# Performance work log

Hardware: AMD Instinct MI355X
Metric: run time of the kernel (lower is better)

Reference implementation:

```python
import jax, jax.numpy as jnp
import numpy as np

D = 768
H = 16
DH = D // H  # 48
SCALE = 1.0 / np.sqrt(DH).astype(np.float32)
EPS = 1e-3  # keras LayerNormalization default epsilon
NEG = -1e9


def setup_inputs() -> dict:
    key = jax.random.key(0)
    ks = jax.random.split(key, 10)
    B, S = 4, 2048
    q = jax.random.normal(ks[0], (B, S, D), dtype=jnp.float32)
    k = jax.random.normal(ks[1], (B, S, D), dtype=jnp.float32)
    v = jax.random.normal(ks[2], (B, S, D), dtype=jnp.float32)
    # Dense projection params (glorot-ish scale)
    w_std = 1.0 / np.sqrt(D)
    Wq = jax.random.normal(ks[3], (D, D), dtype=jnp.float32) * w_std
    Wk = jax.random.normal(ks[4], (D, D), dtype=jnp.float32) * w_std
    Wv = jax.random.normal(ks[5], (D, D), dtype=jnp.float32) * w_std
    bq = jnp.zeros((D,), jnp.float32)
    bk = jnp.zeros((D,), jnp.float32)
    bv = jnp.zeros((D,), jnp.float32)
    gamma = jnp.ones((D,), jnp.float32)
    beta = jnp.zeros((D,), jnp.float32)
    return {"q": q, "k": k, "v": v, "Wq": Wq, "bq": bq, "Wk": Wk, "bk": bk,
            "Wv": Wv, "bv": bv, "gamma": gamma, "beta": beta}


def reference(q, k, v, Wq, bq, Wk, bk, Wv, bv, gamma, beta):
    use_causal = True  # exercise the causal-mask path
    B, S, _ = q.shape
    # Projections, then split into heads (tf.split on last axis == reshape)
    Q = (q @ Wq + bq).reshape(B, S, H, DH)
    K = (k @ Wk + bk).reshape(B, S, H, DH)
    V = (v @ Wv + bv).reshape(B, S, H, DH)
    # scores: [B, H, Sq, Sk]
    scores = jnp.einsum('bqhd,bkhd->bhqk', Q, K) * SCALE
    if use_causal:
        qi = jnp.arange(S)[:, None]
        ki = jnp.arange(S)[None, :]
        mask = jnp.where(qi >= ki, 0.0, NEG).astype(scores.dtype)
        scores = scores + mask
    attn = jax.nn.softmax(scores, axis=-1)
    out = jnp.einsum('bhqk,bkhd->bqhd', attn, V).reshape(B, S, D)
    # LayerNorm over last dim
    mu = jnp.mean(out, axis=-1, keepdims=True)
    var = jnp.mean(jnp.square(out - mu), axis=-1, keepdims=True)
    return (out - mu) * jax.lax.rsqrt(var + EPS) * gamma + beta
```

## Files before the change

kernel.cpp:

```cpp
#include <hip/hip_runtime.h>
#include <hip/hip_bf16.h>


#define DMODEL 768
#define NHEAD  16
#define DHEAD  48
#define SEQ    2048
#define NBATCH 4
#define NROWS  (NBATCH * SEQ)
#define QSCALE (0.14433756729740643f * 1.4426950408889634f)

typedef __bf16 bf16x8 __attribute__((ext_vector_type(8)));
typedef float  f32x4  __attribute__((ext_vector_type(4)));

__global__ __launch_bounds__(256) void prep(
    const float* __restrict__ Wq,
    const float* __restrict__ Wk,
    const float* __restrict__ Wv,
    const float* __restrict__ xq,
    const float* __restrict__ xk,
    const float* __restrict__ xv,
    __hip_bfloat16* __restrict__ Wt,
    __hip_bfloat16* __restrict__ Xbq,
    __hip_bfloat16* __restrict__ Xbk,
    __hip_bfloat16* __restrict__ Xbv)
{
    int bid = blockIdx.x;
    if (bid < 1728) {
        __shared__ __hip_bfloat16 tile[32][33];
        int mat = bid / 576;
        int t   = bid - mat * 576;
        int tr  = t / 24, tc = t - (t / 24) * 24;
        const float* W = (mat == 0) ? Wq : (mat == 1) ? Wk : Wv;
        __hip_bfloat16* O = Wt + (size_t)mat * DMODEL * DMODEL;
        int tx = threadIdx.x & 31, ty = threadIdx.x >> 5;
#pragma unroll
        for (int i = 0; i < 32; i += 8)
            tile[ty + i][tx] = __float2bfloat16(W[(size_t)(tr * 32 + ty + i) * DMODEL + tc * 32 + tx]);
        __syncthreads();
#pragma unroll
        for (int i = 0; i < 32; i += 8)
            O[(size_t)(tc * 32 + ty + i) * DMODEL + tr * 32 + tx] = tile[tx][ty + i];
    } else {
        int b2  = bid - 1728;
        int mat = b2 / 3072;
        int r   = b2 - mat * 3072;
        const float* X = (mat == 0) ? xq : (mat == 1) ? xk : xv;
        __hip_bfloat16* O = (mat == 0) ? Xbq : (mat == 1) ? Xbk : Xbv;
        size_t off = (size_t)r * 2048 + threadIdx.x * 8;
        float4 f0 = *(const float4*)(X + off);
        float4 f1 = *(const float4*)(X + off + 4);
        union { __hip_bfloat16 h[8]; uint4 u; } pk;
        pk.h[0] = __float2bfloat16(f0.x); pk.h[1] = __float2bfloat16(f0.y);
        pk.h[2] = __float2bfloat16(f0.z); pk.h[3] = __float2bfloat16(f0.w);
        pk.h[4] = __float2bfloat16(f1.x); pk.h[5] = __float2bfloat16(f1.y);
        pk.h[6] = __float2bfloat16(f1.z); pk.h[7] = __float2bfloat16(f1.w);
        *(uint4*)(O + off) = pk.u;
    }
}

__global__ __launch_bounds__(512, 4) void qkv_proj(
    const __hip_bfloat16* __restrict__ Xbq,
    const __hip_bfloat16* __restrict__ Xbk,
    const __hip_bfloat16* __restrict__ Xbv,
    const __hip_bfloat16* __restrict__ Wt,
    const float* __restrict__ bq,
    const float* __restrict__ bk,
    const float* __restrict__ bv,
    __hip_bfloat16* __restrict__ Qr,
    __hip_bfloat16* __restrict__ Kr,
    __hip_bfloat16* __restrict__ Vt)
{
    __shared__ __hip_bfloat16 Abuf[3][8192];
    __shared__ __hip_bfloat16 Bbuf[2][4096];

    int tid  = threadIdx.x;
    int w    = tid >> 6, lane = tid & 63;
    int l16  = lane & 15, quad = lane >> 4;
    int wm   = w >> 1, wn = w & 1;

    int xcd = blockIdx.x & 7, s = blockIdx.x >> 3;
    int nt  = s % 6;
    int idx = (s / 6) * 8 + xcd;
    int mat = idx >> 5, mt = idx & 31;
    int m0  = mt * 256, n0 = nt * 128;

    const __hip_bfloat16* X = (mat == 0) ? Xbq : (mat == 1) ? Xbk : Xbv;
    const __hip_bfloat16* W = Wt + (size_t)mat * DMODEL * DMODEL;
    const float* bias       = (mat == 0) ? bq : (mat == 1) ? bk : bv;

    int sr = tid >> 2, sc = (tid & 3) * 8;
    const __hip_bfloat16* ga0 = X + (size_t)(m0 + sr) * DMODEL + sc;
    const __hip_bfloat16* ga1 = X + (size_t)(m0 + 128 + sr) * DMODEL + sc;
    const __hip_bfloat16* gb  = W + (size_t)(n0 + sr) * DMODEL + sc;

#define GLD(gp_, lp_) __builtin_amdgcn_global_load_lds(                        \
        (const __attribute__((address_space(1))) void*)(gp_),                  \
        (__attribute__((address_space(3))) void*)(lp_), 16, 0, 0)

    int aoff = (wm * 64 + l16) * 32 + quad * 8;
    int boff = (wn * 64 + l16) * 32 + quad * 8;

    f32x4 acc[4][4] = {};

    GLD(gb,       &Bbuf[0][tid * 8]);
    GLD(ga0,      &Abuf[0][tid * 8]);
    GLD(ga1,      &Abuf[0][4096 + tid * 8]);
    GLD(ga0 + 32, &Abuf[1][tid * 8]);
    GLD(ga1 + 32, &Abuf[1][4096 + tid * 8]);
    asm volatile("s_waitcnt vmcnt(2)" ::: "memory");
    asm volatile("s_barrier" ::: "memory");

    int abuf = 0, bbuf = 0, abS = 2;
    const __hip_bfloat16* gbS  = gb  + 32;
    const __hip_bfloat16* ga0S = ga0 + 64;
    const __hip_bfloat16* ga1S = ga1 + 64;

    for (int kt = 0; kt < 24; ++kt) {
        const __hip_bfloat16* LA = Abuf[abuf];
        const __hip_bfloat16* LB = Bbuf[bbuf];

        bf16x8 a[4], bA[2];
#pragma unroll
        for (int m_ = 0; m_ < 4; ++m_)
            a[m_] = *(const bf16x8*)&LA[aoff + m_ * 512];
        bA[0] = *(const bf16x8*)&LB[boff];
        bA[1] = *(const bf16x8*)&LB[boff + 512];

        if (kt < 23) { GLD(gbS, &Bbuf[bbuf ^ 1][tid * 8]); gbS += 32; }
        if (kt < 22) {
            GLD(ga0S, &Abuf[abS][tid * 8]);
            GLD(ga1S, &Abuf[abS][4096 + tid * 8]);
            ga0S += 32; ga1S += 32;
        }

        asm volatile("s_barrier" ::: "memory");
        __builtin_amdgcn_s_setprio(1);
#pragma unroll
        for (int m_ = 0; m_ < 4; ++m_) {
            acc[m_][0] = __builtin_amdgcn_mfma_f32_16x16x32_bf16(a[m_], bA[0], acc[m_][0], 0, 0, 0);
            acc[m_][1] = __builtin_amdgcn_mfma_f32_16x16x32_bf16(a[m_], bA[1], acc[m_][1], 0, 0, 0);
        }
        __builtin_amdgcn_s_setprio(0);
        asm volatile("s_barrier" ::: "memory");

        bf16x8 bB[2];
        bB[0] = *(const bf16x8*)&LB[boff + 1024];
        bB[1] = *(const bf16x8*)&LB[boff + 1536];

        if (kt < 22) asm volatile("s_waitcnt vmcnt(2)" ::: "memory");
        else         asm volatile("s_waitcnt vmcnt(0)" ::: "memory");
        asm volatile("s_barrier" ::: "memory");
        __builtin_amdgcn_s_setprio(1);
#pragma unroll
        for (int m_ = 0; m_ < 4; ++m_) {
            acc[m_][2] = __builtin_amdgcn_mfma_f32_16x16x32_bf16(a[m_], bB[0], acc[m_][2], 0, 0, 0);
            acc[m_][3] = __builtin_amdgcn_mfma_f32_16x16x32_bf16(a[m_], bB[1], acc[m_][3], 0, 0, 0);
        }
        __builtin_amdgcn_s_setprio(0);
        asm volatile("s_barrier" ::: "memory");

        abuf = (abuf == 2) ? 0 : abuf + 1;
        abS  = (abS  == 2) ? 0 : abS  + 1;
        bbuf ^= 1;
    }
#undef GLD

#pragma unroll
    for (int j = 0; j < 4; ++j) {
        int col = n0 + wn * 64 + j * 16 + l16;
        float bc = bias[col];
        if (mat == 0) {
#pragma unroll
            for (int i = 0; i < 4; ++i) {
                int row0 = m0 + wm * 64 + i * 16 + quad * 4;
#pragma unroll
                for (int r = 0; r < 4; ++r)
                    Qr[(size_t)(row0 + r) * DMODEL + col] =
                        __float2bfloat16((acc[i][j][r] + bc) * QSCALE);
            }
        } else if (mat == 1) {
#pragma unroll
            for (int i = 0; i < 4; ++i) {
                int row0 = m0 + wm * 64 + i * 16 + quad * 4;
#pragma unroll
                for (int r = 0; r < 4; ++r)
                    Kr[(size_t)(row0 + r) * DMODEL + col] =
                        __float2bfloat16(acc[i][j][r] + bc);
            }
        } else {
            int h = col / 48, dh = col - h * 48;
#pragma unroll
            for (int i = 0; i < 4; ++i) {
                int row0 = m0 + wm * 64 + i * 16 + quad * 4;
                int bb = row0 >> 11, s0 = row0 & 2047;
                ushort4 pk;
                union { __hip_bfloat16 b; unsigned short u; } cv;
                cv.b = __float2bfloat16(acc[i][j][0] + bc); pk.x = cv.u;
                cv.b = __float2bfloat16(acc[i][j][1] + bc); pk.y = cv.u;
                cv.b = __float2bfloat16(acc[i][j][2] + bc); pk.z = cv.u;
                cv.b = __float2bfloat16(acc[i][j][3] + bc); pk.w = cv.u;
                *(ushort4*)(Vt + ((size_t)(bb * NHEAD + h) * DHEAD + dh) * SEQ + s0) = pk;
            }
        }
    }
}

__global__ __launch_bounds__(256, 3) void attn(
    const __hip_bfloat16* __restrict__ Qr,
    const __hip_bfloat16* __restrict__ Kr,
    const __hip_bfloat16* __restrict__ Vt,
    __hip_bfloat16* __restrict__ Ao)
{
    __shared__ __hip_bfloat16 Ks[2][64][72];
    __shared__ __hip_bfloat16 Vs[2][48][72];
    __shared__ __hip_bfloat16 Ps[4][32][72];

    int tid  = threadIdx.x;
    int w    = tid >> 6, lane = tid & 63;
    int l16  = lane & 15, quad = lane >> 4;
    int bh   = blockIdx.x & 63;
    int qt   = 15 - (blockIdx.x >> 6);
    int q0   = qt * 128;
    int b    = bh >> 4, h = bh & 15;
    size_t rowbase = (size_t)b * SEQ;

    const __hip_bfloat16* Qp = Qr + rowbase * DMODEL + h * DHEAD;
    const __hip_bfloat16* Kp = Kr + rowbase * DMODEL + h * DHEAD;
    const __hip_bfloat16* Vp = Vt + (size_t)bh * DHEAD * SEQ;

    for (int idx = tid; idx < 1024; idx += 256) {
        int buf = idx >> 9, r = (idx >> 3) & 63, c = idx & 7;
        ((unsigned int*)&Ks[buf][r][48])[c] = 0u;
    }

    bf16x8 bQ0[2], bQ1[2];
#pragma unroll
    for (int i = 0; i < 2; ++i) {
        int qrow = q0 + w * 32 + i * 16 + l16;
        bQ0[i] = *(const bf16x8*)(Qp + (size_t)qrow * DMODEL + quad * 8);
        bQ1[i] = (bf16x8){};
        if (quad < 2)
            bQ1[i] = *(const bf16x8*)(Qp + (size_t)qrow * DMODEL + 32 + quad * 8);
    }

    int rK = tid >> 2, oK = (tid & 3) * 12;
    int dV = tid >> 3, oV = (tid & 7) * 8;

    uint2 kr0, kr1, kr2; uint4 vr0, vr1;

#define ATTN_LOAD(kt_) {                                                        \
        int k0_ = (kt_) * 64;                                                   \
        const __hip_bfloat16* kb_ = Kp + (size_t)(k0_ + rK) * DMODEL + oK;      \
        kr0 = *(const uint2*)(kb_);                                             \
        kr1 = *(const uint2*)(kb_ + 4);                                         \
        kr2 = *(const uint2*)(kb_ + 8);                                         \
        vr0 = *(const uint4*)(Vp + (size_t)dV * SEQ + k0_ + oV);                \
        if (tid < 128) vr1 = *(const uint4*)(Vp + (size_t)(32 + dV) * SEQ + k0_ + oV); }

#define ATTN_STORE(buf_) {                                                      \
        __hip_bfloat16* kd_ = &Ks[buf_][rK][oK];                                \
        *(uint2*)(kd_)     = kr0;                                               \
        *(uint2*)(kd_ + 4) = kr1;                                               \
        *(uint2*)(kd_ + 8) = kr2;                                               \
        *(uint4*)&Vs[buf_][dV][oV] = vr0;                                       \
        if (tid < 128) *(uint4*)&Vs[buf_][32 + dV][oV] = vr1; }

    f32x4 O[2][3] = {};
    float lsum[2] = {0.f, 0.f};

    int ktmax = 2 * qt + 1;
    ATTN_LOAD(0);
    ATTN_STORE(0);
    if (ktmax >= 1) ATTN_LOAD(1);
    __syncthreads();

    for (int kt = 0; kt <= ktmax; ++kt) {
        int buf = kt & 1;
        int k0  = kt * 64;
        if (kt + 1 <= ktmax) ATTN_STORE(buf ^ 1);
        if (kt + 2 <= ktmax) ATTN_LOAD(kt + 2);

        bf16x8 aK0[4], aK1[4];
#pragma unroll
        for (int t = 0; t < 4; ++t) {
            aK0[t] = *(const bf16x8*)&Ks[buf][16 * t + l16][quad * 8];
            aK1[t] = *(const bf16x8*)&Ks[buf][16 * t + l16][32 + quad * 8];
        }

#pragma unroll
        for (int i = 0; i < 2; ++i) {
            int qbase = q0 + w * 32 + i * 16;
            if (k0 > qbase + 15) continue;

            f32x4 s[4];
#pragma unroll
            for (int t = 0; t < 4; ++t) {
                f32x4 z = {};
                z    = __builtin_amdgcn_mfma_f32_16x16x32_bf16(aK0[t], bQ0[i], z, 0, 0, 0);
                s[t] = __builtin_amdgcn_mfma_f32_16x16x32_bf16(aK1[t], bQ1[i], z, 0, 0, 0);
            }

            if (k0 + 63 > qbase) {
                int qg = qbase + l16;
#pragma unroll
                for (int t = 0; t < 4; ++t) {
                    int kg = k0 + 16 * t + quad * 4;
#pragma unroll
                    for (int r = 0; r < 4; ++r)
                        if (kg + r > qg) s[t][r] = -1e30f;
                }
            }

            float ls = 0.f;
#pragma unroll
            for (int t = 0; t < 4; ++t) {
                float p0 = exp2f(s[t][0]), p1 = exp2f(s[t][1]);
                float p2 = exp2f(s[t][2]), p3 = exp2f(s[t][3]);
                ls += (p0 + p1) + (p2 + p3);
                union { __bf16 hv[4]; uint2 u2; } pk;
                pk.hv[0] = (__bf16)p0; pk.hv[1] = (__bf16)p1;
                pk.hv[2] = (__bf16)p2; pk.hv[3] = (__bf16)p3;
                *(uint2*)&Ps[w][i * 16 + l16][16 * t + quad * 4] = pk.u2;
            }
            lsum[i] += ls;
        }

        bf16x8 bV0[3], bV1[3];
#pragma unroll
        for (int dt = 0; dt < 3; ++dt) {
            bV0[dt] = *(const bf16x8*)&Vs[buf][dt * 16 + l16][quad * 8];
            bV1[dt] = *(const bf16x8*)&Vs[buf][dt * 16 + l16][32 + quad * 8];
        }

#pragma unroll
        for (int i = 0; i < 2; ++i) {
            int qbase = q0 + w * 32 + i * 16;
            if (k0 > qbase + 15) continue;
            bf16x8 aP0 = *(const bf16x8*)&Ps[w][i * 16 + l16][quad * 8];
            bf16x8 aP1 = *(const bf16x8*)&Ps[w][i * 16 + l16][32 + quad * 8];
#pragma unroll
            for (int dt = 0; dt < 3; ++dt) {
                O[i][dt] = __builtin_amdgcn_mfma_f32_16x16x32_bf16(aP0, bV0[dt], O[i][dt], 0, 0, 0);
                O[i][dt] = __builtin_amdgcn_mfma_f32_16x16x32_bf16(aP1, bV1[dt], O[i][dt], 0, 0, 0);
            }
        }

        asm volatile("s_waitcnt lgkmcnt(0)" ::: "memory");
        __builtin_amdgcn_s_barrier();
        asm volatile("" ::: "memory");
    }

#pragma unroll
    for (int i = 0; i < 2; ++i) {
        lsum[i] += __shfl_xor(lsum[i], 16, 64);
        lsum[i] += __shfl_xor(lsum[i], 32, 64);
    }

#pragma unroll
    for (int i = 0; i < 2; ++i) {
#pragma unroll
        for (int r = 0; r < 4; ++r) {
            float linv = 1.f / __shfl(lsum[i], quad * 4 + r, 64);
            size_t g = (rowbase + q0 + w * 32 + i * 16 + quad * 4 + r) * DMODEL + h * DHEAD + l16;
            Ao[g + 0]  = __float2bfloat16(O[i][0][r] * linv);
            Ao[g + 16] = __float2bfloat16(O[i][1][r] * linv);
            Ao[g + 32] = __float2bfloat16(O[i][2][r] * linv);
        }
    }
#undef ATTN_LOAD
#undef ATTN_STORE
}

__global__ __launch_bounds__(192) void lnorm(
    const __hip_bfloat16* __restrict__ Ao,
    const float* __restrict__ gamma,
    const float* __restrict__ beta,
    float* __restrict__ out)
{
    __shared__ float rs_[3], rq_[3];
    int row = blockIdx.x;
    int t   = threadIdx.x;
    size_t base = (size_t)row * DMODEL + t * 4;

    ushort4 u = *(const ushort4*)(Ao + base);
    float x0, x1, x2, x3;
    { unsigned int v = (unsigned int)u.x << 16; __builtin_memcpy(&x0, &v, 4); }
    { unsigned int v = (unsigned int)u.y << 16; __builtin_memcpy(&x1, &v, 4); }
    { unsigned int v = (unsigned int)u.z << 16; __builtin_memcpy(&x2, &v, 4); }
    { unsigned int v = (unsigned int)u.w << 16; __builtin_memcpy(&x3, &v, 4); }

    float s = x0 + x1 + x2 + x3;
    float q = x0 * x0 + x1 * x1 + x2 * x2 + x3 * x3;
#pragma unroll
    for (int m = 32; m >= 1; m >>= 1) {
        s += __shfl_xor(s, m, 64);
        q += __shfl_xor(q, m, 64);
    }
    int wv = t >> 6;
    if ((t & 63) == 0) { rs_[wv] = s; rq_[wv] = q; }
    __syncthreads();
    float ts = rs_[0] + rs_[1] + rs_[2];
    float tq = rq_[0] + rq_[1] + rq_[2];
    float mu  = ts * (1.f / 768.f);
    float var = tq * (1.f / 768.f) - mu * mu;
    float rstd = rsqrtf(var + 1e-3f);

    float4 g  = *(const float4*)(gamma + t * 4);
    float4 be = *(const float4*)(beta + t * 4);
    float4 o;
    o.x = (x0 - mu) * rstd * g.x + be.x;
    o.y = (x1 - mu) * rstd * g.y + be.y;
    o.z = (x2 - mu) * rstd * g.z + be.z;
    o.w = (x3 - mu) * rstd * g.w + be.w;
    *(float4*)(out + base) = o;
}

extern "C" void kernel_launch(void* const* d_in, const int* in_sizes, int n_in,
                              void* d_out, int out_size, void* d_ws, size_t ws_size,
                              hipStream_t stream) {
    const float* q     = (const float*)d_in[0];
    const float* k     = (const float*)d_in[1];
    const float* v     = (const float*)d_in[2];
    const float* Wq    = (const float*)d_in[3];
    const float* bq    = (const float*)d_in[4];
    const float* Wk    = (const float*)d_in[5];
    const float* bk    = (const float*)d_in[6];
    const float* Wv    = (const float*)d_in[7];
    const float* bv    = (const float*)d_in[8];
    const float* gamma = (const float*)d_in[9];
    const float* beta  = (const float*)d_in[10];

    char* basep = (char*)d_ws;
    __hip_bfloat16* Wt = (__hip_bfloat16*)basep;
    __hip_bfloat16* Qr = (__hip_bfloat16*)(basep + 3538944);
    __hip_bfloat16* Kr = Qr + (size_t)NROWS * DMODEL;
    __hip_bfloat16* Vt = Kr + (size_t)NROWS * DMODEL;
    __hip_bfloat16* Ao = Vt + (size_t)NROWS * DMODEL;
    float* out = (float*)d_out;

    __hip_bfloat16* Xbq = (__hip_bfloat16*)d_out;
    __hip_bfloat16* Xbk = Xbq + (size_t)NROWS * DMODEL;
    __hip_bfloat16* Xbv = Ao;

    hipLaunchKernelGGL(prep, dim3(10944), dim3(256), 0, stream,
                       Wq, Wk, Wv, q, k, v, Wt, Xbq, Xbk, Xbv);
    hipLaunchKernelGGL(qkv_proj, dim3(576), dim3(512), 0, stream,
                       Xbq, Xbk, Xbv, Wt, bq, bk, bv, Qr, Kr, Vt);
    hipLaunchKernelGGL(attn, dim3(1024), dim3(256), 0, stream, Qr, Kr, Vt, Ao);
    hipLaunchKernelGGL(lnorm, dim3(8192), dim3(192), 0, stream, Ao, gamma, beta, out);
}
```

Measured before the change: 256.3 us.

## Swizzle attention LDS tiles and pass softmax probabilities via lane shuffles

Drops the padded K/V shared-memory tiles in favour of XOR-swizzled 64-column layouts loaded with full 16-byte accesses. The P tile now moves from the score MFMA output layout into the PV operand layout through cross-lane shuffles, so the per-warp Ps LDS buffer and its round trip go away. The smaller LDS footprint lets launch bounds rise to 4 blocks per CU, and s_setprio is placed around the MFMA groups. The risks are extra shuffle/select instructions, more register pressure under the tighter occupancy bound, and the chance that the swizzle or lane permutation indexing is wrong.

```diff
diff --git a/kernel.cpp b/kernel.cpp
--- a/kernel.cpp
+++ b/kernel.cpp
@@ -206,19 +206,19 @@
     }
 }
 
-__global__ __launch_bounds__(256, 3) void attn(
+__global__ __launch_bounds__(256, 4) void attn(
     const __hip_bfloat16* __restrict__ Qr,
     const __hip_bfloat16* __restrict__ Kr,
     const __hip_bfloat16* __restrict__ Vt,
     __hip_bfloat16* __restrict__ Ao)
 {
-    __shared__ __hip_bfloat16 Ks[2][64][72];
-    __shared__ __hip_bfloat16 Vs[2][48][72];
-    __shared__ __hip_bfloat16 Ps[4][32][72];
+    __shared__ __hip_bfloat16 Ks[2][64][64];
+    __shared__ __hip_bfloat16 Vs[2][48][64];
 
     int tid  = threadIdx.x;
     int w    = tid >> 6, lane = tid & 63;
     int l16  = lane & 15, quad = lane >> 4;
+    bool b1  = (quad & 2) != 0, b0 = (quad & 1) != 0;
     int bh   = blockIdx.x & 63;
     int qt   = 15 - (blockIdx.x >> 6);
     int q0   = qt * 128;
@@ -229,9 +229,9 @@
     const __hip_bfloat16* Kp = Kr + rowbase * DMODEL + h * DHEAD;
     const __hip_bfloat16* Vp = Vt + (size_t)bh * DHEAD * SEQ;
 
-    for (int idx = tid; idx < 1024; idx += 256) {
-        int buf = idx >> 9, r = (idx >> 3) & 63, c = idx & 7;
-        ((unsigned int*)&Ks[buf][r][48])[c] = 0u;
+    {
+        int zbuf = tid >> 7, zr = (tid >> 1) & 63, zsl = 6 + (tid & 1);
+        *(uint4*)&Ks[zbuf][zr][(zsl ^ (zr & 7)) * 8] = (uint4){0u, 0u, 0u, 0u};
     }
 
     bf16x8 bQ0[2], bQ1[2];
@@ -244,30 +244,40 @@
             bQ1[i] = *(const bf16x8*)(Qp + (size_t)qrow * DMODEL + 32 + quad * 8);
     }
 
-    int rK = tid >> 2, oK = (tid & 3) * 12;
-    int dV = tid >> 3, oV = (tid & 7) * 8;
-
-    uint2 kr0, kr1, kr2; uint4 vr0, vr1;
+    int kr1 = tid / 6,          ksl1 = tid - kr1 * 6;
+    int kr2 = (tid + 256) / 6,  ksl2 = (tid + 256) - kr2 * 6;
+    int vd1 = tid >> 3,         vsl1 = tid & 7;
+    int vd2 = (tid + 256) >> 3, vsl2 = tid & 7;
+    int kso1 = (ksl1 ^ (kr1 & 7)) * 8;
+    int kso2 = (ksl2 ^ (kr2 & 7)) * 8;
+    int vso1 = (vsl1 ^ (vd1 & 7)) * 8;
+    int vso2 = (vsl2 ^ (vd2 & 7)) * 8;
+
+    uint4 kv1, kv2, vv1, vv2;
 
 #define ATTN_LOAD(kt_) {                                                        \
         int k0_ = (kt_) * 64;                                                   \
-        const __hip_bfloat16* kb_ = Kp + (size_t)(k0_ + rK) * DMODEL + oK;      \
-        kr0 = *(const uint2*)(kb_);                                             \
-        kr1 = *(const uint2*)(kb_ + 4);                                         \
-        kr2 = *(const uint2*)(kb_ + 8);                                         \
-        vr0 = *(const uint4*)(Vp + (size_t)dV * SEQ + k0_ + oV);                \
-        if (tid < 128) vr1 = *(const uint4*)(Vp + (size_t)(32 + dV) * SEQ + k0_ + oV); }
+        kv1 = *(const uint4*)(Kp + (size_t)(k0_ + kr1) * DMODEL + ksl1 * 8);    \
+        vv1 = *(const uint4*)(Vp + (size_t)vd1 * SEQ + k0_ + vsl1 * 8);         \
+        if (tid < 128) {                                                        \
+            kv2 = *(const uint4*)(Kp + (size_t)(k0_ + kr2) * DMODEL + ksl2 * 8);\
+            vv2 = *(const uint4*)(Vp + (size_t)vd2 * SEQ + k0_ + vsl2 * 8);     \
+        } }
 
 #define ATTN_STORE(buf_) {                                                      \
-        __hip_bfloat16* kd_ = &Ks[buf_][rK][oK];                                \
-        *(uint2*)(kd_)     = kr0;                                               \
-        *(uint2*)(kd_ + 4) = kr1;                                               \
-        *(uint2*)(kd_ + 8) = kr2;                                               \
-        *(uint4*)&Vs[buf_][dV][oV] = vr0;                                       \
-        if (tid < 128) *(uint4*)&Vs[buf_][32 + dV][oV] = vr1; }
+        *(uint4*)&Ks[buf_][kr1][kso1] = kv1;                                    \
+        *(uint4*)&Vs[buf_][vd1][vso1] = vv1;                                    \
+        if (tid < 128) {                                                        \
+            *(uint4*)&Ks[buf_][kr2][kso2] = kv2;                                \
+            *(uint4*)&Vs[buf_][vd2][vso2] = vv2;                                \
+        } }
 
     f32x4 O[2][3] = {};
     float lsum[2] = {0.f, 0.f};
+    const f32x4 zf = {};
+
+    int sA0 = (quad ^ (l16 & 7)) * 8;
+    int sA1 = ((quad + 4) ^ (l16 & 7)) * 8;
 
     int ktmax = 2 * qt + 1;
     ATTN_LOAD(0);
@@ -284,8 +294,14 @@
         bf16x8 aK0[4], aK1[4];
 #pragma unroll
         for (int t = 0; t < 4; ++t) {
-            aK0[t] = *(const bf16x8*)&Ks[buf][16 * t + l16][quad * 8];
-            aK1[t] = *(const bf16x8*)&Ks[buf][16 * t + l16][32 + quad * 8];
+            aK0[t] = *(const bf16x8*)&Ks[buf][16 * t + l16][sA0];
+            aK1[t] = *(const bf16x8*)&Ks[buf][16 * t + l16][sA1];
+        }
+        bf16x8 bV0[3], bV1[3];
+#pragma unroll
+        for (int dt = 0; dt < 3; ++dt) {
+            bV0[dt] = *(const bf16x8*)&Vs[buf][dt * 16 + l16][sA0];
+            bV1[dt] = *(const bf16x8*)&Vs[buf][dt * 16 + l16][sA1];
         }
 
 #pragma unroll
@@ -294,12 +310,13 @@
             if (k0 > qbase + 15) continue;
 
             f32x4 s[4];
+            __builtin_amdgcn_s_setprio(1);
 #pragma unroll
             for (int t = 0; t < 4; ++t) {
-                f32x4 z = {};
-                z    = __builtin_amdgcn_mfma_f32_16x16x32_bf16(aK0[t], bQ0[i], z, 0, 0, 0);
-                s[t] = __builtin_amdgcn_mfma_f32_16x16x32_bf16(aK1[t], bQ1[i], z, 0, 0, 0);
-            }
+                f32x4 z = __builtin_amdgcn_mfma_f32_16x16x32_bf16(aK0[t], bQ0[i], zf, 0, 0, 0);
+                s[t]    = __builtin_amdgcn_mfma_f32_16x16x32_bf16(aK1[t], bQ1[i], z,  0, 0, 0);
+            }
+            __builtin_amdgcn_s_setprio(0);
 
             if (k0 + 63 > qbase) {
                 int qg = qbase + l16;
@@ -313,37 +330,45 @@
             }
 
             float ls = 0.f;
+            unsigned int u_[4][2];
 #pragma unroll
             for (int t = 0; t < 4; ++t) {
                 float p0 = exp2f(s[t][0]), p1 = exp2f(s[t][1]);
                 float p2 = exp2f(s[t][2]), p3 = exp2f(s[t][3]);
                 ls += (p0 + p1) + (p2 + p3);
-                union { __bf16 hv[4]; uint2 u2; } pk;
-                pk.hv[0] = (__bf16)p0; pk.hv[1] = (__bf16)p1;
-                pk.hv[2] = (__bf16)p2; pk.hv[3] = (__bf16)p3;
-                *(uint2*)&Ps[w][i * 16 + l16][16 * t + quad * 4] = pk.u2;
+                union { __hip_bfloat16 hh[2]; unsigned int ww; } pa, pb;
+                pa.hh[0] = __float2bfloat16(p0); pa.hh[1] = __float2bfloat16(p1);
+                pb.hh[0] = __float2bfloat16(p2); pb.hh[1] = __float2bfloat16(p3);
+                u_[t][0] = pa.ww; u_[t][1] = pb.ww;
             }
             lsum[i] += ls;
-        }
-
-        bf16x8 bV0[3], bV1[3];
-#pragma unroll
-        for (int dt = 0; dt < 3; ++dt) {
-            bV0[dt] = *(const bf16x8*)&Vs[buf][dt * 16 + l16][quad * 8];
-            bV1[dt] = *(const bf16x8*)&Vs[buf][dt * 16 + l16][32 + quad * 8];
-        }
-
-#pragma unroll
-        for (int i = 0; i < 2; ++i) {
-            int qbase = q0 + w * 32 + i * 16;
-            if (k0 > qbase + 15) continue;
-            bf16x8 aP0 = *(const bf16x8*)&Ps[w][i * 16 + l16][quad * 8];
-            bf16x8 aP1 = *(const bf16x8*)&Ps[w][i * 16 + l16][32 + quad * 8];
+
+            unsigned int rA0 = __shfl_xor(b1 ? u_[0][0] : u_[1][0], 32, 64);
+            unsigned int rA1 = __shfl_xor(b1 ? u_[0][1] : u_[1][1], 32, 64);
+            unsigned int rB0 = __shfl_xor(b1 ? u_[2][0] : u_[3][0], 32, 64);
+            unsigned int rB1 = __shfl_xor(b1 ? u_[2][1] : u_[3][1], 32, 64);
+            unsigned int X00 = b1 ? rA0 : u_[0][0], X01 = b1 ? rA1 : u_[0][1];
+            unsigned int X10 = b1 ? u_[1][0] : rA0, X11 = b1 ? u_[1][1] : rA1;
+            unsigned int X20 = b1 ? rB0 : u_[2][0], X21 = b1 ? rB1 : u_[2][1];
+            unsigned int X30 = b1 ? u_[3][0] : rB0, X31 = b1 ? u_[3][1] : rB1;
+            unsigned int rC0 = __shfl_xor(b0 ? X00 : X10, 16, 64);
+            unsigned int rC1 = __shfl_xor(b0 ? X01 : X11, 16, 64);
+            unsigned int rD0 = __shfl_xor(b0 ? X20 : X30, 16, 64);
+            unsigned int rD1 = __shfl_xor(b0 ? X21 : X31, 16, 64);
+
+            union { unsigned int ww[4]; bf16x8 v; } P0u, P1u;
+            P0u.ww[0] = b0 ? rC0 : X00;  P0u.ww[1] = b0 ? rC1 : X01;
+            P0u.ww[2] = b0 ? X10 : rC0;  P0u.ww[3] = b0 ? X11 : rC1;
+            P1u.ww[0] = b0 ? rD0 : X20;  P1u.ww[1] = b0 ? rD1 : X21;
+            P1u.ww[2] = b0 ? X30 : rD0;  P1u.ww[3] = b0 ? X31 : rD1;
+
+            __builtin_amdgcn_s_setprio(1);
 #pragma unroll
             for (int dt = 0; dt < 3; ++dt) {
-                O[i][dt] = __builtin_amdgcn_mfma_f32_16x16x32_bf16(aP0, bV0[dt], O[i][dt], 0, 0, 0);
-                O[i][dt] = __builtin_amdgcn_mfma_f32_16x16x32_bf16(aP1, bV1[dt], O[i][dt], 0, 0, 0);
-            }
+                O[i][dt] = __builtin_amdgcn_mfma_f32_16x16x32_bf16(P0u.v, bV0[dt], O[i][dt], 0, 0, 0);
+                O[i][dt] = __builtin_amdgcn_mfma_f32_16x16x32_bf16(P1u.v, bV1[dt], O[i][dt], 0, 0, 0);
+            }
+            __builtin_amdgcn_s_setprio(0);
         }
 
         asm volatile("s_waitcnt lgkmcnt(0)" ::: "memory");
```

Result: slower. 386.3 us (+50.8%).
